# Optimization experiments

Hardware: AMD Instinct MI355X
Metric: run time of the kernel (lower is better)

Reference implementation:

```python
import jax, jax.numpy as jnp
import numpy as np

NUM_HEADS = 16
DIM_HEAD = 64
SCALE = DIM_HEAD ** -0.5
ROPE_BASE = 10000.0


def _rope(t):
    # t: [b, h, n, d] -> rotary embedding with rotate-half convention
    n, d = t.shape[2], t.shape[3]
    inv_freq = 1.0 / (ROPE_BASE ** (jnp.arange(0, d, 2, dtype=jnp.float32) / d))
    freqs = jnp.arange(n, dtype=jnp.float32)[:, None] * inv_freq[None, :]  # [n, d/2]
    cos = jnp.concatenate([jnp.cos(freqs), jnp.cos(freqs)], axis=-1)  # [n, d]
    sin = jnp.concatenate([jnp.sin(freqs), jnp.sin(freqs)], axis=-1)
    t1, t2 = jnp.split(t, 2, axis=-1)
    rot = jnp.concatenate([-t2, t1], axis=-1)
    return t * cos + rot * sin


def setup_inputs() -> dict:
    key = jax.random.key(0)
    k1, k2, k3 = jax.random.split(key, 3)
    B, N, D = 2, 2049, 1024  # 2048 patches + 1 cls token
    x = jax.random.normal(k1, (B, N, D), dtype=jnp.float32)
    ln_gamma = jnp.ones((D,), dtype=jnp.float32)
    ln_beta = jnp.zeros((D,), dtype=jnp.float32)
    w_qkv = jax.random.normal(k2, (D, 3 * NUM_HEADS * DIM_HEAD), dtype=jnp.float32) * 0.02
    w_out = jax.random.normal(k3, (NUM_HEADS * DIM_HEAD, D), dtype=jnp.float32) * 0.02
    return {"x": x, "ln_gamma": ln_gamma, "ln_beta": ln_beta, "w_qkv": w_qkv, "w_out": w_out}


def reference(x, ln_gamma, ln_beta, w_qkv, w_out):
    B, N, D = x.shape
    # LayerNorm (eps=1e-5, torch default)
    mu = jnp.mean(x, axis=-1, keepdims=True)
    var = jnp.mean(jnp.square(x - mu), axis=-1, keepdims=True)
    xn = (x - mu) * jax.lax.rsqrt(var + 1e-5) * ln_gamma + ln_beta
    # QKV projection (no bias)
    qkv = xn @ w_qkv  # [B, N, 3*H*Dh]
    q, k, v = jnp.split(qkv, 3, axis=-1)
    def to_heads(t):
        return t.reshape(B, N, NUM_HEADS, DIM_HEAD).transpose(0, 2, 1, 3)  # [B,H,N,Dh]
    q, k, v = to_heads(q), to_heads(k), to_heads(v)
    # cls token excluded from RoPE
    q = jnp.concatenate([q[:, :, :1, :], _rope(q[:, :, 1:, :])], axis=2)
    k = jnp.concatenate([k[:, :, :1, :], _rope(k[:, :, 1:, :])], axis=2)
    dots = jnp.einsum('bhqd,bhkd->bhqk', q, k) * SCALE
    attn = jax.nn.softmax(dots, axis=-1)
    out = jnp.einsum('bhqk,bhkd->bhqd', attn, v)
    out = out.transpose(0, 2, 1, 3).reshape(B, N, NUM_HEADS * DIM_HEAD)
    return out @ w_out
```

## Files before the change

### kernel.cpp

```cpp
#include <hip/hip_runtime.h>

#define B_    2
#define N_    2049
#define NPAD  2112
#define D_    1024
#define H_    16
#define DH    64
#define MROWS (B_ * N_)
#define MPAD  4224
#define QSCALE 0.18033688011117674f

using bf16x8 = __attribute__((ext_vector_type(8))) short;
using f32x4  = __attribute__((ext_vector_type(4))) float;
using f32x16 = __attribute__((ext_vector_type(16))) float;

#define AS1 __attribute__((address_space(1)))
#define AS3 __attribute__((address_space(3)))

__device__ __forceinline__ float bf2f(short s) {
  union { unsigned u; float f; } a; a.u = ((unsigned)(unsigned short)s) << 16; return a.f;
}
__device__ __forceinline__ short f2bf(float f) {
  union { float f; unsigned u; } a; a.f = f;
  unsigned r = a.u + 0x7fffu + ((a.u >> 16) & 1u);
  return (short)(r >> 16);
}
__device__ __forceinline__ unsigned pack_trunc(float lo, float hi) {
  union { float f; unsigned u; } a, b; a.f = lo; b.f = hi;
  return (b.u & 0xffff0000u) | (a.u >> 16);
}
__device__ __forceinline__ float hexp2(float x) { return __builtin_amdgcn_exp2f(x); }
__device__ __forceinline__ void dma16(const short* g, AS3 short* l) {
  __builtin_amdgcn_global_load_lds((const AS1 unsigned*)g, (AS3 unsigned*)l, 16, 0, 0);
}

__global__ __launch_bounds__(256) void prep_kernel(const float* __restrict__ x,
                                                   const float* __restrict__ gamma,
                                                   const float* __restrict__ beta,
                                                   short* __restrict__ xn,
                                                   const float* __restrict__ w_qkv,
                                                   short* __restrict__ wqkvT,
                                                   const float* __restrict__ w_out,
                                                   short* __restrict__ woutT) {
  int blk = blockIdx.x;
  int tid = threadIdx.x;
  __shared__ float T[64][65];
  __shared__ float sb[4], s2b[4];

  if (blk < MROWS) {
    int row = blk;
    const float4 v = ((const float4*)(x + (size_t)row * D_))[tid];
    float s  = v.x + v.y + v.z + v.w;
    float ss = v.x * v.x + v.y * v.y + v.z * v.z + v.w * v.w;
    for (int o = 1; o < 64; o <<= 1) { s += __shfl_xor(s, o, 64); ss += __shfl_xor(ss, o, 64); }
    int wid = tid >> 6;
    if ((tid & 63) == 0) { sb[wid] = s; s2b[wid] = ss; }
    __syncthreads();
    float st  = sb[0] + sb[1] + sb[2] + sb[3];
    float sst = s2b[0] + s2b[1] + s2b[2] + s2b[3];
    float mu  = st * (1.0f / D_);
    float var = sst * (1.0f / D_) - mu * mu;
    float rs  = rsqrtf(var + 1e-5f);
    const float4 g  = ((const float4*)gamma)[tid];
    const float4 be = ((const float4*)beta)[tid];
    short4 o4;
    o4.x = f2bf((v.x - mu) * rs * g.x + be.x);
    o4.y = f2bf((v.y - mu) * rs * g.y + be.y);
    o4.z = f2bf((v.z - mu) * rs * g.z + be.z);
    o4.w = f2bf((v.w - mu) * rs * g.w + be.w);
    ((short4*)(xn + (size_t)row * D_))[tid] = o4;
    return;
  }

  const float* in; short* out; int K, Nn, t2;
  int b2 = blk - MROWS;
  if (b2 < 768) { in = w_qkv; out = wqkvT; K = 1024; Nn = 3072; t2 = b2; }
  else          { in = w_out; out = woutT; K = 1024; Nn = 1024; t2 = b2 - 768; }
  int k0 = (t2 & 15) * 64;
  int n0 = (t2 >> 4) * 64;
  int r = tid >> 2, c0 = (tid & 3) * 16;
  const float* ip = in + (size_t)(k0 + r) * Nn + n0 + c0;
  #pragma unroll
  for (int j = 0; j < 4; ++j) {
    float4 v = *(const float4*)(ip + j * 4);
    T[r][c0 + j * 4 + 0] = v.x; T[r][c0 + j * 4 + 1] = v.y;
    T[r][c0 + j * 4 + 2] = v.z; T[r][c0 + j * 4 + 3] = v.w;
  }
  __syncthreads();
  bf16x8 w0, w1;
  #pragma unroll
  for (int j = 0; j < 8; ++j) {
    w0[j] = f2bf(T[c0 + j][r]);
    w1[j] = f2bf(T[c0 + 8 + j][r]);
  }
  short* op = out + (size_t)(n0 + r) * K + k0 + c0;
  *(bf16x8*)op = w0;
  *(bf16x8*)(op + 8) = w1;
}

#define BM 128
#define BK 32
template <typename OutT>
__global__ __launch_bounds__(256) void gemm128(const short* __restrict__ A,
                                               const short* __restrict__ BT,
                                               OutT* __restrict__ C,
                                               int Mstore, int Ncols, int K) {
  int lane = threadIdx.x & 63, wid = threadIdx.x >> 6;
  int quad = lane >> 4, l16 = lane & 15;
  int wr = wid >> 1, wc = wid & 1;
  int m0 = blockIdx.x * BM;
  int n0 = blockIdx.y * BM;

  __shared__ __align__(16) short Abuf[2][BM * BK];
  __shared__ __align__(16) short Bbuf[2][BM * BK];
  AS3 short* AbufL = (AS3 short*)&Abuf[0][0];
  AS3 short* BbufL = (AS3 short*)&Bbuf[0][0];

  f32x4 acc[4][4] = {};

  int lrow = lane >> 2, lcol8 = (lane & 3) * 8;
  const short* Ag = A  + (size_t)(m0 + lrow) * K + lcol8;
  const short* Bg = BT + (size_t)(n0 + lrow) * K + lcol8;

  auto stage = [&](int kt, int bb) {
    int k0 = kt * BK;
    #pragma unroll
    for (int i = 0; i < 2; ++i) {
      int j = wid * 2 + i;
      dma16(Ag + (size_t)j * 16 * K + k0, AbufL + bb * (BM * BK) + j * 512);
      dma16(Bg + (size_t)j * 16 * K + k0, BbufL + bb * (BM * BK) + j * 512);
    }
  };

  stage(0, 0);
  __syncthreads();

  int KT = K / BK;
  for (int kt = 0; kt < KT; ++kt) {
    int cur = kt & 1;
    if (kt + 1 < KT) stage(kt + 1, cur ^ 1);
    const short* Ab = &Abuf[cur][0];
    const short* Bb = &Bbuf[cur][0];
    bf16x8 af[4], bfr[4];
    #pragma unroll
    for (int s = 0; s < 4; ++s)
      af[s] = *(const bf16x8*)&Ab[(wr * 64 + s * 16 + l16) * BK + quad * 8];
    #pragma unroll
    for (int t = 0; t < 4; ++t)
      bfr[t] = *(const bf16x8*)&Bb[(wc * 64 + t * 16 + l16) * BK + quad * 8];
    #pragma unroll
    for (int s = 0; s < 4; ++s)
      #pragma unroll
      for (int t = 0; t < 4; ++t)
        acc[s][t] = __builtin_amdgcn_mfma_f32_16x16x32_bf16(af[s], bfr[t], acc[s][t], 0, 0, 0);
    __syncthreads();
  }

  #pragma unroll
  for (int s = 0; s < 4; ++s)
    #pragma unroll
    for (int r = 0; r < 4; ++r) {
      int row = m0 + wr * 64 + s * 16 + quad * 4 + r;
      if (row < Mstore) {
        size_t rb = (size_t)row * Ncols + n0 + wc * 64;
        #pragma unroll
        for (int t = 0; t < 4; ++t) {
          float val = acc[s][t][r];
          if constexpr (sizeof(OutT) == 2)
            C[rb + t * 16 + l16] = (OutT)(unsigned short)f2bf(val);
          else
            C[rb + t * 16 + l16] = (OutT)val;
        }
      }
    }
}

__global__ __launch_bounds__(256) void rope_kernel(const short* __restrict__ qkv,
                                                   short* __restrict__ qg,
                                                   short* __restrict__ kfrag,
                                                   short* __restrict__ vfrag) {
  int bh = blockIdx.y;
  int n0 = blockIdx.x * 64;
  int b = bh >> 4, h = bh & 15;
  int t = threadIdx.x;
  int nl = t >> 2;
  int p  = t & 3;
  int n  = n0 + nl;
  size_t hb = (size_t)bh * NPAD * DH;
  size_t ob = hb + (size_t)n * DH;

  __shared__ short Vt[64][66];
  __shared__ short Kt[64][66];

  bf16x8 oq1 = {}, oq2 = {}, ok1 = {}, ok2 = {};
  short v1s[8] = {}, v2s[8] = {};
  if (n < N_) {
    size_t ib = ((size_t)(b * N_ + n)) * 3072 + h * DH;
    bf16x8 q1v = *(const bf16x8*)(qkv + ib + p * 8);
    bf16x8 q2v = *(const bf16x8*)(qkv + ib + 32 + p * 8);
    bf16x8 k1v = *(const bf16x8*)(qkv + ib + 1024 + p * 8);
    bf16x8 k2v = *(const bf16x8*)(qkv + ib + 1024 + 32 + p * 8);
    bf16x8 v1v = *(const bf16x8*)(qkv + ib + 2048 + p * 8);
    bf16x8 v2v = *(const bf16x8*)(qkv + ib + 2048 + 32 + p * 8);
    #pragma unroll
    for (int j = 0; j < 8; ++j) {
      int i = p * 8 + j;
      float q1 = bf2f(q1v[j]), q2 = bf2f(q2v[j]);
      float k1 = bf2f(k1v[j]), k2 = bf2f(k2v[j]);
      if (n > 0) {
        float ang = (float)(n - 1) * hexp2((float)i * -0.4152410118609203f);
        float rev = ang * 0.15915494309189535f;
        rev = rev - floorf(rev);
        float sn = __builtin_amdgcn_sinf(rev);
        float cs = __builtin_amdgcn_cosf(rev);
        float nq1 = q1 * cs - q2 * sn, nq2 = q2 * cs + q1 * sn;
        float nk1 = k1 * cs - k2 * sn, nk2 = k2 * cs + k1 * sn;
        q1 = nq1; q2 = nq2; k1 = nk1; k2 = nk2;
      }
      oq1[j] = f2bf(q1 * QSCALE); oq2[j] = f2bf(q2 * QSCALE);
      ok1[j] = f2bf(k1); ok2[j] = f2bf(k2);
      v1s[j] = v1v[j]; v2s[j] = v2v[j];
    }
  }
  *(bf16x8*)(qg + ob + p * 8)      = oq1;
  *(bf16x8*)(qg + ob + 32 + p * 8) = oq2;
  #pragma unroll
  for (int j = 0; j < 8; ++j) {
    Vt[nl][p * 8 + j]      = v1s[j];
    Vt[nl][32 + p * 8 + j] = v2s[j];
    Kt[nl][p * 8 + j]      = ok1[j];
    Kt[nl][32 + p * 8 + j] = ok2[j];
  }
  __syncthreads();

  int l = t & 63, c = t >> 6;
  int lk = l & 31, hi = l >> 5;
  size_t tb = hb + (size_t)(n0 >> 6) * 4096;
  bf16x8 wv0, wv1, wk0, wk1;
  #pragma unroll
  for (int i = 0; i < 8; ++i) {
    int keyr = c * 16 + hi * 8 + i;
    wv0[i] = Vt[keyr][lk];
    wv1[i] = Vt[keyr][32 + lk];
    wk0[i] = Kt[lk][keyr];
    wk1[i] = Kt[32 + lk][keyr];
  }
  *(bf16x8*)(vfrag + tb + (size_t)(0 * 4 + c) * 512 + l * 8) = wv0;
  *(bf16x8*)(vfrag + tb + (size_t)(4 + c) * 512 + l * 8)     = wv1;
  *(bf16x8*)(kfrag + tb + (size_t)(0 * 4 + c) * 512 + l * 8) = wk0;
  *(bf16x8*)(kfrag + tb + (size_t)(4 + c) * 512 + l * 8)     = wk1;
}

__global__ __launch_bounds__(256, 3) void attn_kernel(const short* __restrict__ qg,
                                                      const short* __restrict__ kfrag,
                                                      const short* __restrict__ vfrag,
                                                      short* __restrict__ Opart,
                                                      float* __restrict__ lpart) {
  int blk = blockIdx.x;
  int xcd = blk & 7;
  int t_  = blk >> 3;
  int bh  = xcd * 4 + (t_ & 3);
  int u   = t_ >> 2;
  int ks  = (u >= 17) ? 1 : 0;
  int qblk = u - ks * 17;
  int kt0 = ks * 17, kt1 = ks ? 32 : 16;

  int lane = threadIdx.x & 63, wid = threadIdx.x >> 6;
  int q    = lane & 31;
  int half = lane >> 5;
  int q0   = qblk * 128 + wid * 32;
  size_t hb = (size_t)bh * NPAD * DH;
  const short* kf_hb = kfrag + hb;
  const short* vf_hb = vfrag + hb;

  __shared__ __align__(16) short Kbuf[3][8 * 512];
  AS3 short* KbufL = (AS3 short*)&Kbuf[0][0];
  const short* KbufR = &Kbuf[0][0];

  int qr = q0 + q; if (qr >= NPAD) qr = 0;
  const short* qp = qg + hb + (size_t)qr * DH + half * 8;
  bf16x8 qf[4];
  #pragma unroll
  for (int s = 0; s < 4; ++s) qf[s] = *(const bf16x8*)(qp + s * 16);

  f32x16 o0 = {}, o1 = {};
  float lrun = 0.0f;

  auto stage = [&](int kt, int bb) {
    const short* src = kf_hb + (size_t)kt * 4096;
    #pragma unroll
    for (int i = 0; i < 2; ++i) {
      int j = wid * 2 + i;
      dma16(src + j * 512 + lane * 8, KbufL + bb * 4096 + j * 512);
    }
  };

  stage(kt0, 0);
  stage(kt0 + 1, 1);

  for (int kt = kt0; kt <= kt1; ++kt) {
    int rb = (kt - kt0) % 3;
    int k0 = kt * 64;

    asm volatile("s_waitcnt vmcnt(2)" ::: "memory");
    __builtin_amdgcn_s_barrier();

    const short* vt = vf_hb + (size_t)kt * 4096;
    bf16x8 vf0[4], vf1[4];
    #pragma unroll
    for (int s = 0; s < 4; ++s) {
      vf0[s] = *(const bf16x8*)(vt + (0 * 4 + s) * 512 + lane * 8);
      vf1[s] = *(const bf16x8*)(vt + (4 + s) * 512 + lane * 8);
    }
    __builtin_amdgcn_sched_barrier(0);
    if (kt + 2 <= kt1) stage(kt + 2, (kt - kt0 + 2) % 3);
    __builtin_amdgcn_sched_barrier(0);

    const short* Kc = KbufR + rb * 4096;
    f32x16 sA = {}, sB = {};
    __builtin_amdgcn_s_setprio(1);
    #pragma unroll
    for (int s = 0; s < 4; ++s) {
      bf16x8 kf0 = *(const bf16x8*)&Kc[(0 * 4 + s) * 512 + lane * 8];
      bf16x8 kf1 = *(const bf16x8*)&Kc[(1 * 4 + s) * 512 + lane * 8];
      sA = __builtin_amdgcn_mfma_f32_32x32x16_bf16(kf0, qf[s], sA, 0, 0, 0);
      sB = __builtin_amdgcn_mfma_f32_32x32x16_bf16(kf1, qf[s], sB, 0, 0, 0);
    }
    __builtin_amdgcn_s_setprio(0);

    if (k0 + 64 > N_) {
      #pragma unroll
      for (int rr = 0; rr < 16; ++rr) {
        int key = (rr & 3) + 8 * (rr >> 2) + 4 * half;
        if (k0 + key >= N_)      sA[rr] = -1e30f;
        if (k0 + 32 + key >= N_) sB[rr] = -1e30f;
      }
    }

    float vsum = 0.0f;
    #pragma unroll
    for (int rr = 0; rr < 16; ++rr) {
      sA[rr] = hexp2(sA[rr]); vsum += sA[rr];
      sB[rr] = hexp2(sB[rr]); vsum += sB[rr];
    }
    lrun += vsum;

    unsigned w[4][4];
    #pragma unroll
    for (int g = 0; g < 2; ++g) {
      #pragma unroll
      for (int fs = 0; fs < 2; ++fs) {
        int b0 = fs * 8;
        float e0, e1, e2, e3, e4, e5, e6, e7;
        if (g == 0) {
          e0 = sA[b0+0]; e1 = sA[b0+1]; e2 = sA[b0+2]; e3 = sA[b0+3];
          e4 = sA[b0+4]; e5 = sA[b0+5]; e6 = sA[b0+6]; e7 = sA[b0+7];
        } else {
          e0 = sB[b0+0]; e1 = sB[b0+1]; e2 = sB[b0+2]; e3 = sB[b0+3];
          e4 = sB[b0+4]; e5 = sB[b0+5]; e6 = sB[b0+6]; e7 = sB[b0+7];
        }
        unsigned X1 = pack_trunc(e0, e1);
        unsigned X2 = pack_trunc(e2, e3);
        unsigned Y1 = pack_trunc(e4, e5);
        unsigned Y2 = pack_trunc(e6, e7);
        asm("v_permlane32_swap_b32 %0, %1" : "+v"(X1), "+v"(Y1));
        asm("v_permlane32_swap_b32 %0, %1" : "+v"(X2), "+v"(Y2));
        int kst = g * 2 + fs;
        w[kst][0] = X1; w[kst][1] = X2; w[kst][2] = Y1; w[kst][3] = Y2;
      }
    }

    __builtin_amdgcn_s_setprio(1);
    #pragma unroll
    for (int kst = 0; kst < 4; ++kst) {
      union { unsigned u[4]; bf16x8 v; } bw;
      bw.u[0] = w[kst][0]; bw.u[1] = w[kst][1]; bw.u[2] = w[kst][2]; bw.u[3] = w[kst][3];
      o0 = __builtin_amdgcn_mfma_f32_32x32x16_bf16(vf0[kst], bw.v, o0, 0, 0, 0);
      o1 = __builtin_amdgcn_mfma_f32_32x32x16_bf16(vf1[kst], bw.v, o1, 0, 0, 0);
    }
    __builtin_amdgcn_s_setprio(0);
  }

  lrun += __shfl_xor(lrun, 32, 64);

  int qrow = q0 + q;
  if (qrow < N_) {
    size_t ob = (((size_t)ks * 32 + bh) * NPAD + qrow) * 64;
    #pragma unroll
    for (int m = 0; m < 2; ++m) {
      #pragma unroll
      for (int gq = 0; gq < 4; ++gq) {
        float a0 = m ? o1[gq*4+0] : o0[gq*4+0];
        float a1 = m ? o1[gq*4+1] : o0[gq*4+1];
        float a2 = m ? o1[gq*4+2] : o0[gq*4+2];
        float a3 = m ? o1[gq*4+3] : o0[gq*4+3];
        short4 st;
        st.x = f2bf(a0); st.y = f2bf(a1); st.z = f2bf(a2); st.w = f2bf(a3);
        int dh = m * 32 + gq * 8 + half * 4;
        *(short4*)(Opart + ob + dh) = st;
      }
    }
    if (half == 0) lpart[((size_t)ks * 32 + bh) * NPAD + qrow] = lrun;
  }
}

__global__ __launch_bounds__(256) void combine_kernel(const short* __restrict__ Opart,
                                                      const float* __restrict__ lpart,
                                                      short* __restrict__ attn_out) {
  int idx = blockIdx.x * 256 + threadIdx.x;
  const int total = 32 * N_ * 16;
  if (idx >= total) return;
  int c4 = idx & 15;
  int t = idx >> 4;
  int n = t % N_;
  int bh = t / N_;
  int b = bh >> 4, h = bh & 15;
  const size_t halfO = (size_t)32 * NPAD * 64;
  size_t off = ((size_t)bh * NPAD + n) * 64 + c4 * 4;
  short4 a  = *(const short4*)(Opart + off);
  short4 bb = *(const short4*)(Opart + halfO + off);
  float la = lpart[(size_t)bh * NPAD + n];
  float lb = lpart[(size_t)32 * NPAD + (size_t)bh * NPAD + n];
  float inv = 1.0f / (la + lb);
  short4 st;
  st.x = f2bf((bf2f(a.x) + bf2f(bb.x)) * inv);
  st.y = f2bf((bf2f(a.y) + bf2f(bb.y)) * inv);
  st.z = f2bf((bf2f(a.z) + bf2f(bb.z)) * inv);
  st.w = f2bf((bf2f(a.w) + bf2f(bb.w)) * inv);
  size_t rowb = ((size_t)(b * N_ + n)) * (H_ * DH) + h * DH + c4 * 4;
  *(short4*)(attn_out + rowb) = st;
}

extern "C" void kernel_launch(void* const* d_in, const int* in_sizes, int n_in,
                              void* d_out, int out_size, void* d_ws, size_t ws_size,
                              hipStream_t stream) {
  const float* x     = (const float*)d_in[0];
  const float* gamma = (const float*)d_in[1];
  const float* beta  = (const float*)d_in[2];
  const float* w_qkv = (const float*)d_in[3];
  const float* w_out = (const float*)d_in[4];

  short* wqkvT = (short*)d_ws;
  short* woutT = wqkvT + (size_t)3072 * 1024;
  short* xn    = woutT + (size_t)1024 * 1024;
  short* qkv   = xn    + (size_t)MPAD * 1024;
  short* qg    = qkv   + (size_t)MPAD * 3072;
  short* kfragG = qg    + (size_t)B_ * H_ * NPAD * DH;
  short* vfragG = kfragG + (size_t)B_ * H_ * NPAD * DH;
  short* attn_out = xn;
  short* Opart = qkv;
  float* lpart = (float*)(qkv + (size_t)2 * 32 * NPAD * 64);

  prep_kernel<<<MROWS + 768 + 256, 256, 0, stream>>>(x, gamma, beta, xn,
                                                     w_qkv, wqkvT, w_out, woutT);
  {
    dim3 g(MPAD / 128, 3072 / 128);
    gemm128<unsigned short><<<g, 256, 0, stream>>>(xn, wqkvT, (unsigned short*)qkv, MROWS, 3072, 1024);
  }
  {
    dim3 g(33, 32);
    rope_kernel<<<g, 256, 0, stream>>>(qkv, qg, kfragG, vfragG);
  }
  attn_kernel<<<8 * 4 * 17 * 2, 256, 0, stream>>>(qg, kfragG, vfragG, Opart, lpart);
  combine_kernel<<<(32 * N_ * 16 + 255) / 256, 256, 0, stream>>>(Opart, lpart, attn_out);
  {
    dim3 g(MPAD / 128, 1024 / 128);
    gemm128<float><<<g, 256, 0, stream>>>(attn_out, woutT, (float*)d_out, MROWS, 1024, 1024);
  }
}
```

Baseline: 233.0 us.

## Store GEMM operands in pre-tiled block layout for contiguous DMA staging

The producers of GEMM inputs (LayerNorm output, transposed weights, attention combine output) now write in a tiled layout where each 128-row by 32-column tile is contiguous. The GEMM staging loads become fully contiguous 16-byte-per-lane copies instead of strided row reads, which is meant to improve global load coalescing for the LDS DMA path. The producer writes become scattered across tiles, and the consumers must agree on the layout, so it only works if the buffers are padded to multiples of 128 rows.

```diff
diff --git a/kernel.cpp b/kernel.cpp
--- a/kernel.cpp
+++ b/kernel.cpp
@@ -32,6 +32,14 @@
 __device__ __forceinline__ float hexp2(float x) { return __builtin_amdgcn_exp2f(x); }
 __device__ __forceinline__ void dma16(const short* g, AS3 short* l) {
   __builtin_amdgcn_global_load_lds((const AS1 unsigned*)g, (AS3 unsigned*)l, 16, 0, 0);
+}
+
+__device__ __forceinline__ size_t tiled_off(int m, int k) {
+  return ((size_t)(m >> 7) << 17)
+       + (size_t)(((k >> 5) << 12)
+       + ((((m & 127) >> 4)) << 9)
+       + (((((m & 15) << 2) | ((k & 31) >> 3))) << 3)
+       + (k & 7));
 }
 
 __global__ __launch_bounds__(256) void prep_kernel(const float* __restrict__ x,
@@ -68,14 +76,14 @@
     o4.y = f2bf((v.y - mu) * rs * g.y + be.y);
     o4.z = f2bf((v.z - mu) * rs * g.z + be.z);
     o4.w = f2bf((v.w - mu) * rs * g.w + be.w);
-    ((short4*)(xn + (size_t)row * D_))[tid] = o4;
+    *(short4*)(xn + tiled_off(row, tid * 4)) = o4;
     return;
   }
 
-  const float* in; short* out; int K, Nn, t2;
+  const float* in; short* out; int Nn, t2;
   int b2 = blk - MROWS;
-  if (b2 < 768) { in = w_qkv; out = wqkvT; K = 1024; Nn = 3072; t2 = b2; }
-  else          { in = w_out; out = woutT; K = 1024; Nn = 1024; t2 = b2 - 768; }
+  if (b2 < 768) { in = w_qkv; out = wqkvT; Nn = 3072; t2 = b2; }
+  else          { in = w_out; out = woutT; Nn = 1024; t2 = b2 - 768; }
   int k0 = (t2 & 15) * 64;
   int n0 = (t2 >> 4) * 64;
   int r = tid >> 2, c0 = (tid & 3) * 16;
@@ -93,9 +101,8 @@
     w0[j] = f2bf(T[c0 + j][r]);
     w1[j] = f2bf(T[c0 + 8 + j][r]);
   }
-  short* op = out + (size_t)(n0 + r) * K + k0 + c0;
-  *(bf16x8*)op = w0;
-  *(bf16x8*)(op + 8) = w1;
+  *(bf16x8*)(out + tiled_off(n0 + r, k0 + c0))     = w0;
+  *(bf16x8*)(out + tiled_off(n0 + r, k0 + c0 + 8)) = w1;
 }
 
 #define BM 128
@@ -118,17 +125,15 @@
 
   f32x4 acc[4][4] = {};
 
-  int lrow = lane >> 2, lcol8 = (lane & 3) * 8;
-  const short* Ag = A  + (size_t)(m0 + lrow) * K + lcol8;
-  const short* Bg = BT + (size_t)(n0 + lrow) * K + lcol8;
+  const short* Ap = A  + ((size_t)(m0 >> 7) << 17);
+  const short* Bp = BT + ((size_t)(n0 >> 7) << 17);
 
   auto stage = [&](int kt, int bb) {
-    int k0 = kt * BK;
     #pragma unroll
     for (int i = 0; i < 2; ++i) {
       int j = wid * 2 + i;
-      dma16(Ag + (size_t)j * 16 * K + k0, AbufL + bb * (BM * BK) + j * 512);
-      dma16(Bg + (size_t)j * 16 * K + k0, BbufL + bb * (BM * BK) + j * 512);
+      dma16(Ap + ((size_t)kt << 12) + j * 512 + lane * 8, AbufL + bb * (BM * BK) + j * 512);
+      dma16(Bp + ((size_t)kt << 12) + j * 512 + lane * 8, BbufL + bb * (BM * BK) + j * 512);
     }
   };
 
@@ -427,8 +432,7 @@
   st.y = f2bf((bf2f(a.y) + bf2f(bb.y)) * inv);
   st.z = f2bf((bf2f(a.z) + bf2f(bb.z)) * inv);
   st.w = f2bf((bf2f(a.w) + bf2f(bb.w)) * inv);
-  size_t rowb = ((size_t)(b * N_ + n)) * (H_ * DH) + h * DH + c4 * 4;
-  *(short4*)(attn_out + rowb) = st;
+  *(short4*)(attn_out + tiled_off(b * N_ + n, h * DH + c4 * 4)) = st;
 }
 
 extern "C" void kernel_launch(void* const* d_in, const int* in_sizes, int n_in,
```

Result: no change. 231.9 us (-0.5%).
